# Optimization experiments

Hardware: AMD Instinct MI355X
Metric: run time of the kernel (lower is better)

## Reference

```python
import jax, jax.numpy as jnp
import numpy as np

RADIUS = 3
TEMP = 0.1
EPS = 1e-6


def bilinear_resize(x, oh, ow):
    # Matches torch F.interpolate(mode='bilinear', align_corners=False):
    # half-pixel centers, source coord clamped to >= 0, no antialiasing.
    b, c, h, w = x.shape
    ys = jnp.maximum((jnp.arange(oh, dtype=x.dtype) + 0.5) * (h / oh) - 0.5, 0.0)
    xs = jnp.maximum((jnp.arange(ow, dtype=x.dtype) + 0.5) * (w / ow) - 0.5, 0.0)
    y0f = jnp.floor(ys)
    x0f = jnp.floor(xs)
    wy = (ys - y0f)[:, None]          # [oh,1]
    wx = (xs - x0f)[None, :]          # [1,ow]
    y0 = jnp.clip(y0f, 0, h - 1).astype(jnp.int32)
    y1 = jnp.clip(y0f + 1, 0, h - 1).astype(jnp.int32)
    x0 = jnp.clip(x0f, 0, w - 1).astype(jnp.int32)
    x1 = jnp.clip(x0f + 1, 0, w - 1).astype(jnp.int32)
    r0 = x[:, :, y0, :]
    r1 = x[:, :, y1, :]
    v00 = r0[:, :, :, x0]; v01 = r0[:, :, :, x1]
    v10 = r1[:, :, :, x0]; v11 = r1[:, :, :, x1]
    return (1 - wy) * ((1 - wx) * v00 + wx * v01) + wy * ((1 - wx) * v10 + wx * v11)


def setup_inputs() -> dict:
    key = jax.random.key(0)
    k1, k2, k3 = jax.random.split(key, 3)
    fL = jax.random.normal(k1, (4, 256, 96, 320), dtype=jnp.float32)
    fR = jax.random.normal(k2, (4, 256, 96, 320), dtype=jnp.float32)
    disp_full = jax.random.uniform(k3, (4, 1, 384, 1280), dtype=jnp.float32) * 64.0
    return {"fL": fL, "fR": fR, "disp_full": disp_full}


def reference(fL, fR, disp_full):
    B, C, h4, w4 = fL.shape
    H, W = disp_full.shape[-2], disp_full.shape[-1]
    # quarter-res disparity
    disp0 = bilinear_resize(disp_full, h4, w4) / 4.0            # [B,1,h4,w4]
    # cosine correlation volume over 2*radius+1 horizontal shifts
    nL = fL / jnp.clip(jnp.linalg.norm(fL, axis=1, keepdims=True), EPS)
    nR = fR / jnp.clip(jnp.linalg.norm(fR, axis=1, keepdims=True), EPS)
    sims = [jnp.sum(nL * jnp.roll(nR, d, axis=-1), axis=1)
            for d in range(-RADIUS, RADIUS + 1)]
    # original wraps build_cosine_cost in @torch.no_grad()
    cost = jax.lax.stop_gradient(jnp.stack(sims, axis=1))       # [B,7,h4,w4]
    p = jax.nn.softmax(cost / TEMP, axis=1)
    offsets = jnp.arange(-RADIUS, RADIUS + 1, dtype=fL.dtype).reshape(1, -1, 1, 1)
    delta = jnp.sum(p * offsets, axis=1, keepdims=True)          # [B,1,h4,w4]
    disp_ref = disp0 + delta
    conf = jnp.max(p, axis=1, keepdims=True)
    # laplacian smoothing (smooth=True)
    lap = jnp.array([[0., 1., 0.], [1., -4., 1.], [0., 1., 0.]], dtype=fL.dtype).reshape(1, 1, 3, 3)
    lap_out = jax.lax.conv_general_dilated(disp_ref, lap, (1, 1), [(1, 1), (1, 1)])
    disp_q = disp_ref - 0.2 * lap_out
    disp_full_ref = bilinear_resize(disp_q, H, W) * 4.0
    conf_full = bilinear_resize(conf, H, W)
    return disp_full_ref, conf_full
```

## Files before the change

### kernel.cpp

```cpp
#include <hip/hip_runtime.h>
#include <math.h>

constexpr int B_ = 4, C_ = 256, H4 = 96, W4 = 320, HF = 384, WF = 1280;
constexpr int CHUNKS = 5;
constexpr float EPSV = 1e-6f;
constexpr int LOW = B_ * H4 * W4;
constexpr int FULL = B_ * HF * WF;

__device__ __forceinline__ void accum_batch(
    const float4 vL, const float4 wA, const float4 wB, const float4 wC,
    const bool rsel, float* __restrict__ acc, float* __restrict__ sL,
    float* __restrict__ sR, float* __restrict__ sH)
{
    const float lv[4]  = {vL.x, vL.y, vL.z, vL.w};
    const float wv[12] = {wA.x, wA.y, wA.z, wA.w,
                          wB.x, wB.y, wB.z, wB.w,
                          wC.x, wC.y, wC.z, wC.w};
#pragma unroll
    for (int k = 0; k < 7; ++k)
#pragma unroll
        for (int p = 0; p < 4; ++p)
            acc[k * 4 + p] = fmaf(lv[p], wv[p + k + 1], acc[k * 4 + p]);
#pragma unroll
    for (int p = 0; p < 4; ++p) {
        sL[p] = fmaf(lv[p], lv[p], sL[p]);
        sR[p] = fmaf(wv[4 + p], wv[4 + p], sR[p]);
    }
#pragma unroll
    for (int j = 0; j < 3; ++j) {
        const float t = rsel ? wv[8 + j] : wv[1 + j];
        sH[j] = fmaf(t, t, sH[j]);
    }
}

__global__ __launch_bounds__(256)
void phase1(const float* __restrict__ fL, const float* __restrict__ fR,
            const float* __restrict__ D, float* __restrict__ dref,
            float* __restrict__ conf)
{
    const int bi = blockIdx.x;
    const int chunk = bi % CHUNKS;
    const int y = (bi / CHUNKS) % H4;
    const int b = bi / (CHUNKS * H4);
    const int tid = threadIdx.x;
    const int wave = tid >> 6;
    const int lane = tid & 63;
    const int q = lane & 15;
    const int csub = lane >> 4;
    const int x0 = chunk * 64;
    const int xo = x0 + 4 * q;

    const size_t chanStride = (size_t)H4 * W4;
    const size_t rowBase = (((size_t)b * C_) * H4 + y) * W4;

    int lx = xo - 4; if (lx < 0)   lx += W4;
    int rx = xo + 4; if (rx >= W4) rx -= W4;

    const int c0 = wave * 64 + csub;
    const float* pL = fL + rowBase + (size_t)c0 * chanStride;
    const float* pR = fR + rowBase + (size_t)c0 * chanStride;
    const size_t step = 4 * chanStride;

    float acc[28];
#pragma unroll
    for (int i = 0; i < 28; ++i) acc[i] = 0.f;
    float sL[4] = {0.f, 0.f, 0.f, 0.f};
    float sR[4] = {0.f, 0.f, 0.f, 0.f};
    float sH[3] = {0.f, 0.f, 0.f};
    const bool rsel = (q == 15);

    float4 bL[3], bA[3], bB[3], bC[3];

#pragma unroll
    for (int g = 0; g < 2; ++g) {
        const size_t o = (size_t)g * step;
        bL[g] = *(const float4*)(pL + o + xo);
        bA[g] = *(const float4*)(pR + o + lx);
        bB[g] = *(const float4*)(pR + o + xo);
        bC[g] = *(const float4*)(pR + o + rx);
    }
    asm volatile("" ::: "memory");

#pragma unroll
    for (int it = 0; it < 16; ++it) {
        const int cur = it % 3;
        if (it + 2 < 16) {
            const int nxt = (it + 2) % 3;
            const size_t o = (size_t)(it + 2) * step;
            bL[nxt] = *(const float4*)(pL + o + xo);
            bA[nxt] = *(const float4*)(pR + o + lx);
            bB[nxt] = *(const float4*)(pR + o + xo);
            bC[nxt] = *(const float4*)(pR + o + rx);
        }
        asm volatile("" ::: "memory");
        accum_batch(bL[cur], bA[cur], bB[cur], bC[cur], rsel, acc, sL, sR, sH);
    }

#pragma unroll
    for (int i = 0; i < 28; ++i) {
        acc[i] += __shfl_xor(acc[i], 16);
        acc[i] += __shfl_xor(acc[i], 32);
    }
#pragma unroll
    for (int p = 0; p < 4; ++p) {
        sL[p] += __shfl_xor(sL[p], 16); sL[p] += __shfl_xor(sL[p], 32);
        sR[p] += __shfl_xor(sR[p], 16); sR[p] += __shfl_xor(sR[p], 32);
    }
#pragma unroll
    for (int j = 0; j < 3; ++j) {
        sH[j] += __shfl_xor(sH[j], 16);
        sH[j] += __shfl_xor(sH[j], 32);
    }

    __shared__ float rec[4][16][37];
    __shared__ float hrec[4][2][3];
    __shared__ float sss[70];
    if (lane < 16) {
#pragma unroll
        for (int i = 0; i < 28; ++i) rec[wave][lane][i] = acc[i];
#pragma unroll
        for (int p = 0; p < 4; ++p) {
            rec[wave][lane][28 + p] = sL[p];
            rec[wave][lane][32 + p] = sR[p];
        }
    }
    if (lane == 0) {
#pragma unroll
        for (int j = 0; j < 3; ++j) hrec[wave][0][j] = sH[j];
    }
    if (lane == 15) {
#pragma unroll
        for (int j = 0; j < 3; ++j) hrec[wave][1][j] = sH[j];
    }
    __syncthreads();

    float D7[7];
    float rsL = 0.f;
    if (tid < 64) {
        const int qq = tid >> 2, pp = tid & 3;
#pragma unroll
        for (int k = 0; k < 7; ++k)
            D7[k] = rec[0][qq][4 * k + pp] + rec[1][qq][4 * k + pp]
                  + rec[2][qq][4 * k + pp] + rec[3][qq][4 * k + pp];
        rsL = rec[0][qq][28 + pp] + rec[1][qq][28 + pp]
            + rec[2][qq][28 + pp] + rec[3][qq][28 + pp];
        const float rsR = rec[0][qq][32 + pp] + rec[1][qq][32 + pp]
                        + rec[2][qq][32 + pp] + rec[3][qq][32 + pp];
        sss[3 + tid] = rsR;
        if (tid < 3)
            sss[tid] = hrec[0][0][tid] + hrec[1][0][tid]
                     + hrec[2][0][tid] + hrec[3][0][tid];
        if (tid >= 61) {
            const int j = tid - 61;
            sss[67 + j] = hrec[0][1][j] + hrec[1][1][j]
                        + hrec[2][1][j] + hrec[3][1][j];
        }
    }
    __syncthreads();

    if (tid < 64) {
        const float nLv = fmaxf(sqrtf(rsL), EPSV);
        float cost[7];
#pragma unroll
        for (int k = 0; k < 7; ++k) {
            const float nR = fmaxf(sqrtf(sss[tid + k]), EPSV);
            cost[6 - k] = (D7[k] / (nLv * nR)) * 10.0f;
        }
        float m = cost[0];
#pragma unroll
        for (int i = 1; i < 7; ++i) m = fmaxf(m, cost[i]);
        float sum = 0.f, dsum = 0.f;
#pragma unroll
        for (int i = 0; i < 7; ++i) {
            const float e = __expf(cost[i] - m);
            sum += e;
            dsum += e * (float)(i - 3);
        }
        const float delta = dsum / sum;
        const float cf = 1.0f / sum;

        const int xpix = x0 + tid;
        const int Y0 = 4 * y + 1, X0 = 4 * xpix + 1;
        const size_t dbase = ((size_t)b * HF + Y0) * WF + X0;
        const float s4 = D[dbase] + D[dbase + 1] + D[dbase + WF] + D[dbase + WF + 1];
        const float disp0 = s4 * 0.0625f;

        const size_t o = ((size_t)b * H4 + y) * W4 + xpix;
        dref[o] = disp0 + delta;
        conf[o] = cf;
    }
}

__device__ __forceinline__ float dq_val(const float* __restrict__ dref,
                                        size_t base, int yq, int xq)
{
    size_t i = base + (size_t)yq * W4 + xq;
    float c  = dref[i];
    float up = (yq > 0)      ? dref[i - W4] : 0.f;
    float dn = (yq < H4 - 1) ? dref[i + W4] : 0.f;
    float lf = (xq > 0)      ? dref[i - 1]  : 0.f;
    float rt = (xq < W4 - 1) ? dref[i + 1]  : 0.f;
    return c - 0.2f * (up + dn + lf + rt - 4.f * c);
}

__global__ void phase2(const float* __restrict__ dref, const float* __restrict__ cf,
                       float* __restrict__ out)
{
    const int idx = blockIdx.x * blockDim.x + threadIdx.x;
    constexpr int WQ = WF / 4;
    if (idx >= FULL / 4) return;
    const int k = idx % WQ;
    const int Y = (idx / WQ) % HF;
    const int b = idx / (WQ * HF);

    const float ys = fmaxf((Y + 0.5f) * 0.25f - 0.5f, 0.f);
    const float y0f = floorf(ys);
    const float wy = ys - y0f;
    const int y0 = min((int)y0f, H4 - 1);
    const int y1 = min(y0 + 1, H4 - 1);
    const size_t base = (size_t)b * (H4 * W4);

    const int xa = max(k - 1, 0);
    const int xb = k;
    const int xc = min(k + 1, W4 - 1);

    const float da = (1.f - wy) * dq_val(dref, base, y0, xa) + wy * dq_val(dref, base, y1, xa);
    const float db = (1.f - wy) * dq_val(dref, base, y0, xb) + wy * dq_val(dref, base, y1, xb);
    const float dc = (1.f - wy) * dq_val(dref, base, y0, xc) + wy * dq_val(dref, base, y1, xc);

    const size_t r0 = base + (size_t)y0 * W4;
    const size_t r1 = base + (size_t)y1 * W4;
    const float ca = (1.f - wy) * cf[r0 + xa] + wy * cf[r1 + xa];
    const float cb = (1.f - wy) * cf[r0 + xb] + wy * cf[r1 + xb];
    const float cc = (1.f - wy) * cf[r0 + xc] + wy * cf[r1 + xc];

    float4 dv, cv;
    dv.x = 4.0f * (0.375f * da + 0.625f * db);
    dv.y = 4.0f * (0.125f * da + 0.875f * db);
    dv.z = 4.0f * (0.875f * db + 0.125f * dc);
    dv.w = 4.0f * (0.625f * db + 0.375f * dc);
    cv.x = 0.375f * ca + 0.625f * cb;
    cv.y = 0.125f * ca + 0.875f * cb;
    cv.z = 0.875f * cb + 0.125f * cc;
    cv.w = 0.625f * cb + 0.375f * cc;

    const size_t o = (((size_t)b * HF + Y) * WF) + 4 * k;
    *(float4*)&out[o] = dv;
    *(float4*)&out[(size_t)FULL + o] = cv;
}

extern "C" void kernel_launch(void* const* d_in, const int* in_sizes, int n_in,
                              void* d_out, int out_size, void* d_ws, size_t ws_size,
                              hipStream_t stream)
{
    const float* fL = (const float*)d_in[0];
    const float* fR = (const float*)d_in[1];
    const float* D  = (const float*)d_in[2];
    float* out  = (float*)d_out;
    float* ws   = (float*)d_ws;
    float* dref = ws;
    float* conf = ws + LOW;

    phase1<<<B_ * H4 * CHUNKS, 256, 0, stream>>>(fL, fR, D, dref, conf);
    phase2<<<(FULL / 4 + 255) / 256, 256, 0, stream>>>(dref, conf, out);
}
```

Before: 282.6 us.

## Restructure correlation as channel-split async LDS pipeline with atomic partial sums

```diff
diff --git a/kernel.cpp b/kernel.cpp
--- a/kernel.cpp
+++ b/kernel.cpp
@@ -2,193 +2,155 @@
 #include <math.h>
 
 constexpr int B_ = 4, C_ = 256, H4 = 96, W4 = 320, HF = 384, WF = 1280;
-constexpr int CHUNKS = 5;
 constexpr float EPSV = 1e-6f;
 constexpr int LOW = B_ * H4 * W4;
 constexpr int FULL = B_ * HF * WF;
 
-__device__ __forceinline__ void accum_batch(
-    const float4 vL, const float4 wA, const float4 wB, const float4 wC,
-    const bool rsel, float* __restrict__ acc, float* __restrict__ sL,
-    float* __restrict__ sR, float* __restrict__ sH)
-{
-    const float lv[4]  = {vL.x, vL.y, vL.z, vL.w};
-    const float wv[12] = {wA.x, wA.y, wA.z, wA.w,
-                          wB.x, wB.y, wB.z, wB.w,
-                          wC.x, wC.y, wC.z, wC.w};
+constexpr int CQ  = 4;
+constexpr int CPB = C_ / CQ;
+constexpr int CG  = 2;
+constexpr int NIT = CPB / CG;
+constexpr int NBUF = 4;
+constexpr int BUF_FLOATS = CG * 2 * W4;
+
+__device__ __forceinline__ void async_copy16(const float* g, float* l)
+{
+    __builtin_amdgcn_global_load_lds(
+        (const __attribute__((address_space(1))) void*)g,
+        (__attribute__((address_space(3))) void*)l,
+        16, 0, 0);
+}
+
+__global__ __launch_bounds__(320)
+void phase1(const float* __restrict__ fL, const float* __restrict__ fR,
+            float* __restrict__ P)
+{
+    const int bi = blockIdx.x;
+    const int cq = bi / (B_ * H4);
+    const int r  = bi % (B_ * H4);
+    const int b  = r / H4;
+    const int y  = r % H4;
+    const int tid  = threadIdx.x;
+    const int wave = tid >> 6;
+    const int x = tid;
+
+    const size_t chanStride = (size_t)H4 * W4;
+    const int c0 = cq * CPB;
+
+    __shared__ float lds[NBUF * BUF_FLOATS];
+
+    const int sch  = tid / 160;
+    const int stns = (tid / 80) & 1;
+    const int sxq  = 4 * (tid % 80);
+    const float* const sbase = (stns ? fR : fL)
+        + ((size_t)b * C_ + (c0 + sch)) * chanStride + (size_t)y * W4 + sxq;
+
+    float* const ldswave = &lds[0] + wave * 256;
+
+    int idx[7];
+#pragma unroll
+    for (int k = 0; k < 7; ++k) {
+        int t = x + k - 3;
+        if (t < 0) t += W4; else if (t >= W4) t -= W4;
+        idx[k] = t;
+    }
+
+    float dot[7] = {0.f,0.f,0.f,0.f,0.f,0.f,0.f};
+    float ssL = 0.f, ssR = 0.f;
+
+    async_copy16(sbase,                        ldswave + 0 * BUF_FLOATS);
+    async_copy16(sbase + (size_t)CG * chanStride, ldswave + 1 * BUF_FLOATS);
+
+    auto compute = [&](int g) {
+        const float* bf = &lds[(g & (NBUF - 1)) * BUF_FLOATS];
+#pragma unroll
+        for (int ch = 0; ch < CG; ++ch) {
+            const float* cf = bf + ch * (2 * W4);
+            const float a = cf[x];
+            const float* wr = cf + W4;
+            float w[7];
+#pragma unroll
+            for (int k = 0; k < 7; ++k) w[k] = wr[idx[k]];
+#pragma unroll
+            for (int k = 0; k < 7; ++k) dot[k] = fmaf(a, w[k], dot[k]);
+            ssL = fmaf(a, a, ssL);
+            ssR = fmaf(w[3], w[3], ssR);
+        }
+    };
+
+    for (int g = 0; g < NIT - 2; ++g) {
+        async_copy16(sbase + (size_t)(g + 2) * CG * chanStride,
+                     ldswave + ((g + 2) & (NBUF - 1)) * BUF_FLOATS);
+        asm volatile("s_waitcnt vmcnt(2)" ::: "memory");
+        __builtin_amdgcn_s_barrier();
+        asm volatile("" ::: "memory");
+        compute(g);
+    }
+    asm volatile("s_waitcnt vmcnt(1)" ::: "memory");
+    __builtin_amdgcn_s_barrier();
+    asm volatile("" ::: "memory");
+    compute(NIT - 2);
+    asm volatile("s_waitcnt vmcnt(0)" ::: "memory");
+    __builtin_amdgcn_s_barrier();
+    asm volatile("" ::: "memory");
+    compute(NIT - 1);
+
+    const size_t rowoff = ((size_t)b * H4 + y) * W4 + x;
 #pragma unroll
     for (int k = 0; k < 7; ++k)
-#pragma unroll
-        for (int p = 0; p < 4; ++p)
-            acc[k * 4 + p] = fmaf(lv[p], wv[p + k + 1], acc[k * 4 + p]);
-#pragma unroll
-    for (int p = 0; p < 4; ++p) {
-        sL[p] = fmaf(lv[p], lv[p], sL[p]);
-        sR[p] = fmaf(wv[4 + p], wv[4 + p], sR[p]);
-    }
-#pragma unroll
-    for (int j = 0; j < 3; ++j) {
-        const float t = rsel ? wv[8 + j] : wv[1 + j];
-        sH[j] = fmaf(t, t, sH[j]);
-    }
-}
-
-__global__ __launch_bounds__(256)
-void phase1(const float* __restrict__ fL, const float* __restrict__ fR,
-            const float* __restrict__ D, float* __restrict__ dref,
-            float* __restrict__ conf)
+        atomicAdd(&P[(size_t)k * LOW + rowoff], dot[k]);
+    atomicAdd(&P[(size_t)7 * LOW + rowoff], ssL);
+    atomicAdd(&P[(size_t)8 * LOW + rowoff], ssR);
+}
+
+__global__ __launch_bounds__(320)
+void phase1b(const float* __restrict__ P, const float* __restrict__ D,
+             float* __restrict__ dref, float* __restrict__ conf)
 {
     const int bi = blockIdx.x;
-    const int chunk = bi % CHUNKS;
-    const int y = (bi / CHUNKS) % H4;
-    const int b = bi / (CHUNKS * H4);
-    const int tid = threadIdx.x;
-    const int wave = tid >> 6;
-    const int lane = tid & 63;
-    const int q = lane & 15;
-    const int csub = lane >> 4;
-    const int x0 = chunk * 64;
-    const int xo = x0 + 4 * q;
-
-    const size_t chanStride = (size_t)H4 * W4;
-    const size_t rowBase = (((size_t)b * C_) * H4 + y) * W4;
-
-    int lx = xo - 4; if (lx < 0)   lx += W4;
-    int rx = xo + 4; if (rx >= W4) rx -= W4;
-
-    const int c0 = wave * 64 + csub;
-    const float* pL = fL + rowBase + (size_t)c0 * chanStride;
-    const float* pR = fR + rowBase + (size_t)c0 * chanStride;
-    const size_t step = 4 * chanStride;
-
-    float acc[28];
-#pragma unroll
-    for (int i = 0; i < 28; ++i) acc[i] = 0.f;
-    float sL[4] = {0.f, 0.f, 0.f, 0.f};
-    float sR[4] = {0.f, 0.f, 0.f, 0.f};
-    float sH[3] = {0.f, 0.f, 0.f};
-    const bool rsel = (q == 15);
-
-    float4 bL[3], bA[3], bB[3], bC[3];
-
-#pragma unroll
-    for (int g = 0; g < 2; ++g) {
-        const size_t o = (size_t)g * step;
-        bL[g] = *(const float4*)(pL + o + xo);
-        bA[g] = *(const float4*)(pR + o + lx);
-        bB[g] = *(const float4*)(pR + o + xo);
-        bC[g] = *(const float4*)(pR + o + rx);
-    }
-    asm volatile("" ::: "memory");
-
-#pragma unroll
-    for (int it = 0; it < 16; ++it) {
-        const int cur = it % 3;
-        if (it + 2 < 16) {
-            const int nxt = (it + 2) % 3;
-            const size_t o = (size_t)(it + 2) * step;
-            bL[nxt] = *(const float4*)(pL + o + xo);
-            bA[nxt] = *(const float4*)(pR + o + lx);
-            bB[nxt] = *(const float4*)(pR + o + xo);
-            bC[nxt] = *(const float4*)(pR + o + rx);
-        }
-        asm volatile("" ::: "memory");
-        accum_batch(bL[cur], bA[cur], bB[cur], bC[cur], rsel, acc, sL, sR, sH);
-    }
-
-#pragma unroll
-    for (int i = 0; i < 28; ++i) {
-        acc[i] += __shfl_xor(acc[i], 16);
-        acc[i] += __shfl_xor(acc[i], 32);
-    }
-#pragma unroll
-    for (int p = 0; p < 4; ++p) {
-        sL[p] += __shfl_xor(sL[p], 16); sL[p] += __shfl_xor(sL[p], 32);
-        sR[p] += __shfl_xor(sR[p], 16); sR[p] += __shfl_xor(sR[p], 32);
-    }
-#pragma unroll
-    for (int j = 0; j < 3; ++j) {
-        sH[j] += __shfl_xor(sH[j], 16);
-        sH[j] += __shfl_xor(sH[j], 32);
-    }
-
-    __shared__ float rec[4][16][37];
-    __shared__ float hrec[4][2][3];
-    __shared__ float sss[70];
-    if (lane < 16) {
-#pragma unroll
-        for (int i = 0; i < 28; ++i) rec[wave][lane][i] = acc[i];
-#pragma unroll
-        for (int p = 0; p < 4; ++p) {
-            rec[wave][lane][28 + p] = sL[p];
-            rec[wave][lane][32 + p] = sR[p];
-        }
-    }
-    if (lane == 0) {
-#pragma unroll
-        for (int j = 0; j < 3; ++j) hrec[wave][0][j] = sH[j];
-    }
-    if (lane == 15) {
-#pragma unroll
-        for (int j = 0; j < 3; ++j) hrec[wave][1][j] = sH[j];
-    }
+    const int b = bi / H4, y = bi % H4;
+    const int x = threadIdx.x;
+    const size_t rowoff = (size_t)bi * W4 + x;
+
+    float dot[7];
+#pragma unroll
+    for (int k = 0; k < 7; ++k) dot[k] = P[(size_t)k * LOW + rowoff];
+    const float ssL = P[(size_t)7 * LOW + rowoff];
+    const float ssR = P[(size_t)8 * LOW + rowoff];
+
+    __shared__ float sss[W4];
+    sss[x] = ssR;
     __syncthreads();
 
-    float D7[7];
-    float rsL = 0.f;
-    if (tid < 64) {
-        const int qq = tid >> 2, pp = tid & 3;
-#pragma unroll
-        for (int k = 0; k < 7; ++k)
-            D7[k] = rec[0][qq][4 * k + pp] + rec[1][qq][4 * k + pp]
-                  + rec[2][qq][4 * k + pp] + rec[3][qq][4 * k + pp];
-        rsL = rec[0][qq][28 + pp] + rec[1][qq][28 + pp]
-            + rec[2][qq][28 + pp] + rec[3][qq][28 + pp];
-        const float rsR = rec[0][qq][32 + pp] + rec[1][qq][32 + pp]
-                        + rec[2][qq][32 + pp] + rec[3][qq][32 + pp];
-        sss[3 + tid] = rsR;
-        if (tid < 3)
-            sss[tid] = hrec[0][0][tid] + hrec[1][0][tid]
-                     + hrec[2][0][tid] + hrec[3][0][tid];
-        if (tid >= 61) {
-            const int j = tid - 61;
-            sss[67 + j] = hrec[0][1][j] + hrec[1][1][j]
-                        + hrec[2][1][j] + hrec[3][1][j];
-        }
-    }
-    __syncthreads();
-
-    if (tid < 64) {
-        const float nLv = fmaxf(sqrtf(rsL), EPSV);
-        float cost[7];
-#pragma unroll
-        for (int k = 0; k < 7; ++k) {
-            const float nR = fmaxf(sqrtf(sss[tid + k]), EPSV);
-            cost[6 - k] = (D7[k] / (nLv * nR)) * 10.0f;
-        }
-        float m = cost[0];
-#pragma unroll
-        for (int i = 1; i < 7; ++i) m = fmaxf(m, cost[i]);
-        float sum = 0.f, dsum = 0.f;
-#pragma unroll
-        for (int i = 0; i < 7; ++i) {
-            const float e = __expf(cost[i] - m);
-            sum += e;
-            dsum += e * (float)(i - 3);
-        }
-        const float delta = dsum / sum;
-        const float cf = 1.0f / sum;
-
-        const int xpix = x0 + tid;
-        const int Y0 = 4 * y + 1, X0 = 4 * xpix + 1;
-        const size_t dbase = ((size_t)b * HF + Y0) * WF + X0;
-        const float s4 = D[dbase] + D[dbase + 1] + D[dbase + WF] + D[dbase + WF + 1];
-        const float disp0 = s4 * 0.0625f;
-
-        const size_t o = ((size_t)b * H4 + y) * W4 + xpix;
-        dref[o] = disp0 + delta;
-        conf[o] = cf;
-    }
+    const float nL = fmaxf(sqrtf(ssL), EPSV);
+    float cost[7];
+#pragma unroll
+    for (int k = 0; k < 7; ++k) {
+        int t = x + k - 3;
+        if (t < 0) t += W4; else if (t >= W4) t -= W4;
+        const float nR = fmaxf(sqrtf(sss[t]), EPSV);
+        cost[6 - k] = (dot[k] / (nL * nR)) * 10.0f;
+    }
+    float m = cost[0];
+#pragma unroll
+    for (int i = 1; i < 7; ++i) m = fmaxf(m, cost[i]);
+    float sum = 0.f, dsum = 0.f;
+#pragma unroll
+    for (int i = 0; i < 7; ++i) {
+        const float e = __expf(cost[i] - m);
+        sum += e;
+        dsum += e * (float)(i - 3);
+    }
+    const float delta = dsum / sum;
+    const float cf = 1.0f / sum;
+
+    const int Y0 = 4 * y + 1, X0 = 4 * x + 1;
+    const size_t dbase = ((size_t)b * HF + Y0) * WF + X0;
+    const float s4 = D[dbase] + D[dbase + 1] + D[dbase + WF] + D[dbase + WF + 1];
+    const float disp0 = s4 * 0.0625f;
+
+    dref[rowoff] = disp0 + delta;
+    conf[rowoff] = cf;
 }
 
 __device__ __forceinline__ float dq_val(const float* __restrict__ dref,
@@ -260,7 +222,10 @@
     float* ws   = (float*)d_ws;
     float* dref = ws;
     float* conf = ws + LOW;
-
-    phase1<<<B_ * H4 * CHUNKS, 256, 0, stream>>>(fL, fR, D, dref, conf);
+    float* P    = out;
+
+    hipMemsetAsync(P, 0, (size_t)9 * LOW * sizeof(float), stream);
+    phase1<<<CQ * B_ * H4, 320, 0, stream>>>(fL, fR, P);
+    phase1b<<<B_ * H4, 320, 0, stream>>>(P, D, dref, conf);
     phase2<<<(FULL / 4 + 255) / 256, 256, 0, stream>>>(dref, conf, out);
 }
```

Result: no change. 287.9 us (+1.9%).

## Map one pixel per lane with scalar loads instead of float4 channel-split tiles

Applied to the files above, without the earlier changes.

```diff
diff --git a/kernel.cpp b/kernel.cpp
--- a/kernel.cpp
+++ b/kernel.cpp
@@ -7,33 +7,7 @@
 constexpr int LOW = B_ * H4 * W4;
 constexpr int FULL = B_ * HF * WF;
 
-__device__ __forceinline__ void accum_batch(
-    const float4 vL, const float4 wA, const float4 wB, const float4 wC,
-    const bool rsel, float* __restrict__ acc, float* __restrict__ sL,
-    float* __restrict__ sR, float* __restrict__ sH)
-{
-    const float lv[4]  = {vL.x, vL.y, vL.z, vL.w};
-    const float wv[12] = {wA.x, wA.y, wA.z, wA.w,
-                          wB.x, wB.y, wB.z, wB.w,
-                          wC.x, wC.y, wC.z, wC.w};
-#pragma unroll
-    for (int k = 0; k < 7; ++k)
-#pragma unroll
-        for (int p = 0; p < 4; ++p)
-            acc[k * 4 + p] = fmaf(lv[p], wv[p + k + 1], acc[k * 4 + p]);
-#pragma unroll
-    for (int p = 0; p < 4; ++p) {
-        sL[p] = fmaf(lv[p], lv[p], sL[p]);
-        sR[p] = fmaf(wv[4 + p], wv[4 + p], sR[p]);
-    }
-#pragma unroll
-    for (int j = 0; j < 3; ++j) {
-        const float t = rsel ? wv[8 + j] : wv[1 + j];
-        sH[j] = fmaf(t, t, sH[j]);
-    }
-}
-
-__global__ __launch_bounds__(256)
+__global__ __launch_bounds__(256, 6)
 void phase1(const float* __restrict__ fL, const float* __restrict__ fR,
             const float* __restrict__ D, float* __restrict__ dref,
             float* __restrict__ conf)
@@ -45,115 +19,85 @@
     const int tid = threadIdx.x;
     const int wave = tid >> 6;
     const int lane = tid & 63;
-    const int q = lane & 15;
-    const int csub = lane >> 4;
     const int x0 = chunk * 64;
-    const int xo = x0 + 4 * q;
+    const int x = x0 + lane;
 
     const size_t chanStride = (size_t)H4 * W4;
     const size_t rowBase = (((size_t)b * C_) * H4 + y) * W4;
 
-    int lx = xo - 4; if (lx < 0)   lx += W4;
-    int rx = xo + 4; if (rx >= W4) rx -= W4;
-
-    const int c0 = wave * 64 + csub;
-    const float* pL = fL + rowBase + (size_t)c0 * chanStride;
-    const float* pR = fR + rowBase + (size_t)c0 * chanStride;
-    const size_t step = 4 * chanStride;
-
-    float acc[28];
-#pragma unroll
-    for (int i = 0; i < 28; ++i) acc[i] = 0.f;
-    float sL[4] = {0.f, 0.f, 0.f, 0.f};
-    float sR[4] = {0.f, 0.f, 0.f, 0.f};
+    const float* pL = fL + rowBase + (size_t)(wave * 64) * chanStride;
+    const float* pR = fR + rowBase + (size_t)(wave * 64) * chanStride;
+
+    int xk[7];
+#pragma unroll
+    for (int k = 0; k < 7; ++k) {
+        int t = x + k - 3;
+        if (t < 0) t += W4; else if (t >= W4) t -= W4;
+        xk[k] = t;
+    }
+
+    float dot[7] = {0.f,0.f,0.f,0.f,0.f,0.f,0.f};
+    float ssL = 0.f, ssR = 0.f;
     float sH[3] = {0.f, 0.f, 0.f};
-    const bool rsel = (q == 15);
-
-    float4 bL[3], bA[3], bB[3], bC[3];
-
-#pragma unroll
-    for (int g = 0; g < 2; ++g) {
-        const size_t o = (size_t)g * step;
-        bL[g] = *(const float4*)(pL + o + xo);
-        bA[g] = *(const float4*)(pR + o + lx);
-        bB[g] = *(const float4*)(pR + o + xo);
-        bC[g] = *(const float4*)(pR + o + rx);
-    }
-    asm volatile("" ::: "memory");
-
-#pragma unroll
-    for (int it = 0; it < 16; ++it) {
-        const int cur = it % 3;
-        if (it + 2 < 16) {
-            const int nxt = (it + 2) % 3;
-            const size_t o = (size_t)(it + 2) * step;
-            bL[nxt] = *(const float4*)(pL + o + xo);
-            bA[nxt] = *(const float4*)(pR + o + lx);
-            bB[nxt] = *(const float4*)(pR + o + xo);
-            bC[nxt] = *(const float4*)(pR + o + rx);
-        }
-        asm volatile("" ::: "memory");
-        accum_batch(bL[cur], bA[cur], bB[cur], bC[cur], rsel, acc, sL, sR, sH);
-    }
-
-#pragma unroll
-    for (int i = 0; i < 28; ++i) {
-        acc[i] += __shfl_xor(acc[i], 16);
-        acc[i] += __shfl_xor(acc[i], 32);
-    }
-#pragma unroll
-    for (int p = 0; p < 4; ++p) {
-        sL[p] += __shfl_xor(sL[p], 16); sL[p] += __shfl_xor(sL[p], 32);
-        sR[p] += __shfl_xor(sR[p], 16); sR[p] += __shfl_xor(sR[p], 32);
-    }
-#pragma unroll
-    for (int j = 0; j < 3; ++j) {
-        sH[j] += __shfl_xor(sH[j], 16);
-        sH[j] += __shfl_xor(sH[j], 32);
-    }
-
-    __shared__ float rec[4][16][37];
-    __shared__ float hrec[4][2][3];
+    const bool rsel = (lane == 63);
+
+    float a0 = pL[x];
+    float w0[7];
+#pragma unroll
+    for (int k = 0; k < 7; ++k) w0[k] = pR[xk[k]];
+
+#pragma unroll 2
+    for (int c = 0; c < 64; ++c) {
+        float a1 = 0.f;
+        float w1[7];
+        if (c < 63) {
+            const float* qL = pL + (size_t)(c + 1) * chanStride;
+            const float* qR = pR + (size_t)(c + 1) * chanStride;
+            a1 = qL[x];
+#pragma unroll
+            for (int k = 0; k < 7; ++k) w1[k] = qR[xk[k]];
+        }
+#pragma unroll
+        for (int k = 0; k < 7; ++k) dot[k] = fmaf(a0, w0[k], dot[k]);
+        ssL = fmaf(a0, a0, ssL);
+        ssR = fmaf(w0[3], w0[3], ssR);
+#pragma unroll
+        for (int j = 0; j < 3; ++j) {
+            const float t = rsel ? w0[4 + j] : w0[j];
+            sH[j] = fmaf(t, t, sH[j]);
+        }
+        a0 = a1;
+#pragma unroll
+        for (int k = 0; k < 7; ++k) w0[k] = w1[k];
+    }
+
+    __shared__ float part[256][13];
     __shared__ float sss[70];
-    if (lane < 16) {
-#pragma unroll
-        for (int i = 0; i < 28; ++i) rec[wave][lane][i] = acc[i];
-#pragma unroll
-        for (int p = 0; p < 4; ++p) {
-            rec[wave][lane][28 + p] = sL[p];
-            rec[wave][lane][32 + p] = sR[p];
-        }
-    }
-    if (lane == 0) {
-#pragma unroll
-        for (int j = 0; j < 3; ++j) hrec[wave][0][j] = sH[j];
-    }
-    if (lane == 15) {
-#pragma unroll
-        for (int j = 0; j < 3; ++j) hrec[wave][1][j] = sH[j];
-    }
+#pragma unroll
+    for (int k = 0; k < 7; ++k) part[tid][k] = dot[k];
+    part[tid][7] = ssL;
+    part[tid][8] = ssR;
+#pragma unroll
+    for (int j = 0; j < 3; ++j) part[tid][9 + j] = sH[j];
     __syncthreads();
 
-    float D7[7];
-    float rsL = 0.f;
+    float rdot[7], rsL = 0.f;
     if (tid < 64) {
-        const int qq = tid >> 2, pp = tid & 3;
 #pragma unroll
         for (int k = 0; k < 7; ++k)
-            D7[k] = rec[0][qq][4 * k + pp] + rec[1][qq][4 * k + pp]
-                  + rec[2][qq][4 * k + pp] + rec[3][qq][4 * k + pp];
-        rsL = rec[0][qq][28 + pp] + rec[1][qq][28 + pp]
-            + rec[2][qq][28 + pp] + rec[3][qq][28 + pp];
-        const float rsR = rec[0][qq][32 + pp] + rec[1][qq][32 + pp]
-                        + rec[2][qq][32 + pp] + rec[3][qq][32 + pp];
+            rdot[k] = part[tid][k] + part[tid + 64][k]
+                    + part[tid + 128][k] + part[tid + 192][k];
+        rsL = part[tid][7] + part[tid + 64][7] + part[tid + 128][7] + part[tid + 192][7];
+        const float rsR = part[tid][8] + part[tid + 64][8]
+                        + part[tid + 128][8] + part[tid + 192][8];
         sss[3 + tid] = rsR;
         if (tid < 3)
-            sss[tid] = hrec[0][0][tid] + hrec[1][0][tid]
-                     + hrec[2][0][tid] + hrec[3][0][tid];
+            sss[tid] = part[0][9 + tid] + part[64][9 + tid]
+                     + part[128][9 + tid] + part[192][9 + tid];
         if (tid >= 61) {
             const int j = tid - 61;
-            sss[67 + j] = hrec[0][1][j] + hrec[1][1][j]
-                        + hrec[2][1][j] + hrec[3][1][j];
+            sss[67 + j] = part[63][9 + j] + part[127][9 + j]
+                        + part[191][9 + j] + part[255][9 + j];
         }
     }
     __syncthreads();
@@ -164,7 +108,7 @@
 #pragma unroll
         for (int k = 0; k < 7; ++k) {
             const float nR = fmaxf(sqrtf(sss[tid + k]), EPSV);
-            cost[6 - k] = (D7[k] / (nLv * nR)) * 10.0f;
+            cost[6 - k] = (rdot[k] / (nLv * nR)) * 10.0f;
         }
         float m = cost[0];
 #pragma unroll
```

New measurement: 306.0 us. +8.3%, slower.
